# Kernel tuning notes

Hardware: AMD Instinct MI355X
Metric: run time of the kernel (lower is better)

The kernel has to match this reference:

```python
import jax, jax.numpy as jnp
import numpy as np

NUM_FREQ = 10
HIDDEN = 256
ENC_DIM = 2 * 2 * NUM_FREQ  # input_dim * 2 * num_frequencies = 40
OUT_DIM = 3


def setup_inputs() -> dict:
    key = jax.random.key(0)
    ks = jax.random.split(key, 8)
    B, N = 4, 262144
    x = jax.random.uniform(ks[0], (B, N, 2), dtype=jnp.float32)
    # layer 0: enc_dim -> hidden
    W_in = jax.random.normal(ks[1], (ENC_DIM, HIDDEN), dtype=jnp.float32) * (1.0 / np.sqrt(ENC_DIM))
    b_in = jnp.zeros((HIDDEN,), dtype=jnp.float32)
    # layers 1..6: hidden -> hidden (6 of them)
    W_hid = jax.random.normal(ks[2], (6, HIDDEN, HIDDEN), dtype=jnp.float32) * (1.0 / np.sqrt(HIDDEN))
    b_hid = jnp.zeros((6, HIDDEN), dtype=jnp.float32)
    # layer 7: hidden -> out
    W_out = jax.random.normal(ks[3], (HIDDEN, OUT_DIM), dtype=jnp.float32) * (1.0 / np.sqrt(HIDDEN))
    b_out = jnp.zeros((OUT_DIM,), dtype=jnp.float32)
    return {"x": x, "W_in": W_in, "b_in": b_in, "W_hid": W_hid,
            "b_hid": b_hid, "W_out": W_out, "b_out": b_out}


def _pos_encode(x):
    # x: (B, N, 2) -> (B, N, 40). Matches torch: cat([sin, cos], -1) over freq axis then flatten.
    freq = 2.0 ** jnp.arange(NUM_FREQ, dtype=jnp.float32)  # (10,)
    xe = x[..., :, None] * freq  # (B, N, 2, 10)
    enc = jnp.concatenate([jnp.sin(xe), jnp.cos(xe)], axis=-1)  # (B, N, 2, 20)
    return enc.reshape(x.shape[0], x.shape[1], -1)  # (B, N, 40)


def reference(x, W_in, b_in, W_hid, b_hid, W_out, b_out):
    h = _pos_encode(x)
    h = jax.nn.relu(h @ W_in + b_in)
    for i in range(W_hid.shape[0]):  # 6 hidden layers, fixed small loop
        h = jax.nn.relu(h @ W_hid[i] + b_hid[i])
    out = jnp.tanh(h @ W_out + b_out) / 100.0
    return out
```

## Files before the change

kernel.cpp:

```cpp
#include <hip/hip_runtime.h>
#include <stdint.h>

#define THREADS 256
#define BR      128

#define NG_STRIDE 204800
#define WS_WOUT   819200
#define WS_TOTAL  (WS_WOUT + 16384)


typedef short bf16x8 __attribute__((ext_vector_type(8)));
typedef short bf16x4 __attribute__((ext_vector_type(4)));
typedef float f32x16 __attribute__((ext_vector_type(16)));
typedef float f32x4v __attribute__((ext_vector_type(4)));

__device__ __forceinline__ unsigned short f2bf(float f) {
    union { float f; unsigned int u; } v; v.f = f;
    unsigned int u = v.u;
    u += 0x7fffu + ((u >> 16) & 1u);
    return (unsigned short)(u >> 16);
}
__device__ __forceinline__ unsigned int cvt_pk_bf16(float lo, float hi) {
    unsigned int d;
    asm("v_cvt_pk_bf16_f32 %0, %1, %2" : "=v"(d) : "v"(lo), "v"(hi));
    return d;
}
__device__ __forceinline__ bf16x8 ld_act2(const unsigned char* lo,
                                          const unsigned char* hi) {
    bf16x4 a = *(const bf16x4*)lo;
    bf16x4 b = *(const bf16x4*)hi;
    return __builtin_shufflevector(a, b, 0, 1, 2, 3, 4, 5, 6, 7);
}

__global__ void prep_kernel(const float* __restrict__ W_in,
                            const float* __restrict__ W_hid,
                            const float* __restrict__ W_out,
                            unsigned char* __restrict__ ws) {
    int id = blockIdx.x * 256 + threadIdx.x;
    if (id < 16384) {
        int n = id & 255, k = id >> 8;
        int ng = n >> 6, ft = (n >> 5) & 1, ln = n & 31;
        int kk = k >> 4, hi = (k >> 3) & 1, e = k & 7;
        float v = (k < 40) ? W_in[k * 256 + n] : 0.f;
        *(unsigned short*)(ws + ng * NG_STRIDE + (kk * 2 + ft) * 1024
                           + (hi * 32 + ln) * 16 + e * 2) = f2bf(v);
    } else if (id < 16384 + 393216) {
        int e2 = id - 16384;
        int l = e2 >> 16, r = e2 & 65535;
        int k = r >> 8, n = r & 255;
        int c = k >> 6, kk = (k >> 4) & 3, hi = (k >> 3) & 1, e = k & 7;
        int ng = n >> 6, ft = (n >> 5) & 1, ln = n & 31;
        float v = W_hid[l * 65536 + k * 256 + n];
        *(unsigned short*)(ws + ng * NG_STRIDE + 8192 + l * 32768
                           + ((c * 4 + kk) * 2 + ft) * 1024
                           + (hi * 32 + ln) * 16 + e * 2) = f2bf(v);
    } else if (id < 16384 + 393216 + 8192) {
        int e3 = id - 16384 - 393216;
        int n = e3 >> 8, k = e3 & 255;
        int kk = k >> 4, hi = (k >> 3) & 1, e = k & 7;
        float v = (n < 3) ? W_out[k * 3 + n] : 0.f;
        *(unsigned short*)(ws + WS_WOUT + kk * 1024
                           + (hi * 32 + n) * 16 + e * 2) = f2bf(v);
    }
}

__device__ __forceinline__ void bias_init(const float* __restrict__ bp,
                                          f32x16 (&acc)[2][4], int nblk, int hi) {
    #pragma unroll
    for (int tn = 0; tn < 2; ++tn) {
        #pragma unroll
        for (int g4 = 0; g4 < 4; ++g4) {
            f32x4v bv = *(const f32x4v*)(bp + nblk + tn * 32 + g4 * 8 + hi * 4);
            #pragma unroll
            for (int tr = 0; tr < 4; ++tr) {
                #pragma unroll
                for (int j = 0; j < 4; ++j)
                    acc[tn][tr][g4 * 4 + j] = bv[j];
            }
        }
    }
}

__device__ __forceinline__ void epilogue_frag(f32x16 (&acc)[2][4],
                                              unsigned char* actL,
                                              int vW, int wv) {
    #pragma unroll
    for (int tr = 0; tr < 4; ++tr) {
        #pragma unroll
        for (int tn = 0; tn < 2; ++tn) {
            #pragma unroll
            for (int g4 = 0; g4 < 4; ++g4) {
                float v0 = fmaxf(acc[tn][tr][g4 * 4 + 0], 0.f);
                float v1 = fmaxf(acc[tn][tr][g4 * 4 + 1], 0.f);
                float v2 = fmaxf(acc[tn][tr][g4 * 4 + 2], 0.f);
                float v3 = fmaxf(acc[tn][tr][g4 * 4 + 3], 0.f);
                const int ks  = wv * 4 + tn * 2 + (g4 >> 1);
                const int off = (ks * 4 + tr) * 1024 + ((g4 & 1) << 9);
                uint2 u; u.x = cvt_pk_bf16(v0, v1); u.y = cvt_pk_bf16(v2, v3);
                *(uint2*)&actL[vW + off] = u;
            }
        }
    }
}

__global__ __launch_bounds__(THREADS, 2)
void nerf_main(const float* __restrict__ x,
               const float* __restrict__ b_in,
               const float* __restrict__ b_hid,
               const float* __restrict__ b_out,
               const unsigned char* __restrict__ ws,
               float* __restrict__ out, int nrows) {
    __shared__ __align__(16) unsigned char actL[65536];

    const int tid  = threadIdx.x;
    const int lane = tid & 63;
    const int wv   = tid >> 6;
    const int l31  = lane & 31;
    const int hi   = lane >> 5;
    const int hi16 = hi << 4;
    const int rswz  = (l31 & 15) << 3;
    const int rswz2 = rswz ^ 8;
    const int nblk = wv * 64;
    const int gr0  = blockIdx.x * BR;

    const int vB = lane * 16;
    const int vW = l31 * 16 + hi * 8;

    #pragma unroll
    for (int pass = 0; pass < 2; ++pass) {
        const int rr = (tid >> 2) + pass * 64;
        const int part = tid & 3;
        const int co = part >> 1, hf = part & 1;
        const int grow = gr0 + rr;
        float xv = (grow < nrows) ? x[(size_t)grow * 2 + co] : 0.f;
        const int rowo = rr * 512;
        const int rsw = (rr & 15) << 3;
        const int kb = co * 20 + hf * 10;
        float vv[10];
        #pragma unroll
        for (int f = 0; f < 10; ++f) {
            float ang = xv * (float)(1 << f);
            vv[f] = hf ? __cosf(ang) : __sinf(ang);
        }
        #pragma unroll
        for (int p = 0; p < 5; ++p) {
            unsigned int u = cvt_pk_bf16(vv[2 * p], vv[2 * p + 1]);
            int byte = (kb + 2 * p) * 2;
            *(unsigned int*)&actL[rowo + (byte ^ rsw)] = u;
        }
        int z = 80 + part * 12;
        *(unsigned int*)&actL[rowo + ((z    ) ^ rsw)] = 0u;
        *(unsigned int*)&actL[rowo + ((z + 4) ^ rsw)] = 0u;
        *(unsigned int*)&actL[rowo + ((z + 8) ^ rsw)] = 0u;
    }
    __syncthreads();

    f32x16 acc[2][4];
    const unsigned char* wstream = ws + wv * NG_STRIDE + lane * 16;

    {
        bias_init(b_in, acc, nblk, hi);
        int olo[4], ohi[4];
        #pragma unroll
        for (int kk = 0; kk < 4; ++kk) {
            const int bo = kk * 32 + hi16;
            olo[kk] = l31 * 512 + (bo ^ rswz);
            ohi[kk] = l31 * 512 + (bo ^ rswz2);
        }
        __builtin_amdgcn_s_setprio(1);
        #pragma unroll
        for (int kk = 0; kk < 4; ++kk) {
            const unsigned char* fp = wstream + kk * 2048;
            bf16x8 a0 = *(const bf16x8*)(fp);
            bf16x8 a1 = *(const bf16x8*)(fp + 1024);
            #pragma unroll
            for (int tr = 0; tr < 4; ++tr) {
                bf16x8 b = ld_act2(&actL[olo[kk] + tr * 16384],
                                   &actL[ohi[kk] + tr * 16384]);
                acc[0][tr] = __builtin_amdgcn_mfma_f32_32x32x16_bf16(a0, b, acc[0][tr], 0, 0, 0);
                acc[1][tr] = __builtin_amdgcn_mfma_f32_32x32x16_bf16(a1, b, acc[1][tr], 0, 0, 0);
            }
        }
        __builtin_amdgcn_s_setprio(0);
        __syncthreads();
        epilogue_frag(acc, actL, vW, wv);
        __syncthreads();
        wstream += 8192;
    }

    #pragma unroll 1
    for (int l = 0; l < 6; ++l) {
        bias_init(b_hid + l * 256, acc, nblk, hi);
        __builtin_amdgcn_s_setprio(1);
        #pragma unroll
        for (int c = 0; c < 4; ++c) {
            #pragma unroll
            for (int kk = 0; kk < 4; ++kk) {
                const unsigned char* fp = wstream + (c * 4 + kk) * 2048;
                bf16x8 a0 = *(const bf16x8*)(fp);
                bf16x8 a1 = *(const bf16x8*)(fp + 1024);
                const int fo = (c * 4 + kk) * 4096;
                #pragma unroll
                for (int tr = 0; tr < 4; ++tr) {
                    bf16x8 b = *(const bf16x8*)&actL[vB + fo + tr * 1024];
                    acc[0][tr] = __builtin_amdgcn_mfma_f32_32x32x16_bf16(a0, b, acc[0][tr], 0, 0, 0);
                    acc[1][tr] = __builtin_amdgcn_mfma_f32_32x32x16_bf16(a1, b, acc[1][tr], 0, 0, 0);
                }
            }
        }
        __builtin_amdgcn_s_setprio(0);
        __syncthreads();
        epilogue_frag(acc, actL, vW, wv);
        __syncthreads();
        wstream += 32768;
    }

    {
        f32x16 c0, c1;
        #pragma unroll
        for (int j = 0; j < 16; ++j) { c0[j] = 0.f; c1[j] = 0.f; }
        const unsigned char* wo = ws + WS_WOUT + lane * 16;
        #pragma unroll
        for (int kk = 0; kk < 16; ++kk) {
            bf16x8 a = *(const bf16x8*)(wo + kk * 1024);
            bf16x8 b = *(const bf16x8*)&actL[vB + (kk * 4 + wv) * 1024];
            if (kk & 1) c1 = __builtin_amdgcn_mfma_f32_32x32x16_bf16(a, b, c1, 0, 0, 0);
            else        c0 = __builtin_amdgcn_mfma_f32_32x32x16_bf16(a, b, c0, 0, 0, 0);
        }
        if (hi == 0) {
            const int row = gr0 + wv * 32 + l31;
            if (row < nrows) {
                float* op = out + (size_t)row * 3;
                #pragma unroll
                for (int j = 0; j < 3; ++j)
                    op[j] = tanhf(c0[j] + c1[j] + b_out[j]) * 0.01f;
            }
        }
    }
}

extern "C" void kernel_launch(void* const* d_in, const int* in_sizes, int n_in,
                              void* d_out, int out_size, void* d_ws, size_t ws_size,
                              hipStream_t stream) {
    (void)n_in; (void)out_size;
    const float* x     = (const float*)d_in[0];
    const float* W_in  = (const float*)d_in[1];
    const float* b_in  = (const float*)d_in[2];
    const float* W_hid = (const float*)d_in[3];
    const float* b_hid = (const float*)d_in[4];
    const float* W_out = (const float*)d_in[5];
    const float* b_out = (const float*)d_in[6];
    unsigned char* ws  = (unsigned char*)d_ws;
    float* out = (float*)d_out;

    if (ws_size < (size_t)WS_TOTAL) return;

    const int nrows = in_sizes[0] / 2;
    const int grid  = (nrows + BR - 1) / BR;

    prep_kernel<<<1632, 256, 0, stream>>>(W_in, W_hid, W_out, ws);
    nerf_main<<<grid, THREADS, 0, stream>>>(x, b_in, b_hid, b_out, ws, out, nrows);
}
```

Measured before the change: 716.7 us.

## Use 512-thread blocks of 64 rows with ping-pong activation buffers

Blocks shrink from 128 rows to 64 and grow from 256 to 512 threads. Eight waves split into 4 column groups times 2 row groups, each wave accumulating a single 32-row tile instead of four. Activations alternate between two LDS halves across layers, which removes the barrier before each epilogue. This lowers register pressure (launch bounds 4) for higher occupancy, but each weight fragment fetched from global memory now feeds fewer MFMAs, so per-row weight traffic roughly doubles.

```diff
diff --git a/kernel.cpp b/kernel.cpp
--- a/kernel.cpp
+++ b/kernel.cpp
@@ -1,8 +1,8 @@
 #include <hip/hip_runtime.h>
 #include <stdint.h>
 
-#define THREADS 256
-#define BR      128
+#define THREADS 512
+#define BR      64
 
 #define NG_STRIDE 204800
 #define WS_WOUT   819200
@@ -65,45 +65,65 @@
 }
 
 __device__ __forceinline__ void bias_init(const float* __restrict__ bp,
-                                          f32x16 (&acc)[2][4], int nblk, int hi) {
+                                          f32x16 (&acc)[2], int nblk, int hi) {
     #pragma unroll
     for (int tn = 0; tn < 2; ++tn) {
         #pragma unroll
         for (int g4 = 0; g4 < 4; ++g4) {
             f32x4v bv = *(const f32x4v*)(bp + nblk + tn * 32 + g4 * 8 + hi * 4);
             #pragma unroll
-            for (int tr = 0; tr < 4; ++tr) {
-                #pragma unroll
-                for (int j = 0; j < 4; ++j)
-                    acc[tn][tr][g4 * 4 + j] = bv[j];
-            }
-        }
-    }
-}
-
-__device__ __forceinline__ void epilogue_frag(f32x16 (&acc)[2][4],
+            for (int j = 0; j < 4; ++j)
+                acc[tn][g4 * 4 + j] = bv[j];
+        }
+    }
+}
+
+template <int WBO>
+__device__ __forceinline__ void epilogue_frag(f32x16 (&acc)[2],
                                               unsigned char* actL,
-                                              int vW, int wv) {
+                                              int vW, int ng) {
     #pragma unroll
-    for (int tr = 0; tr < 4; ++tr) {
-        #pragma unroll
-        for (int tn = 0; tn < 2; ++tn) {
-            #pragma unroll
-            for (int g4 = 0; g4 < 4; ++g4) {
-                float v0 = fmaxf(acc[tn][tr][g4 * 4 + 0], 0.f);
-                float v1 = fmaxf(acc[tn][tr][g4 * 4 + 1], 0.f);
-                float v2 = fmaxf(acc[tn][tr][g4 * 4 + 2], 0.f);
-                float v3 = fmaxf(acc[tn][tr][g4 * 4 + 3], 0.f);
-                const int ks  = wv * 4 + tn * 2 + (g4 >> 1);
-                const int off = (ks * 4 + tr) * 1024 + ((g4 & 1) << 9);
-                uint2 u; u.x = cvt_pk_bf16(v0, v1); u.y = cvt_pk_bf16(v2, v3);
-                *(uint2*)&actL[vW + off] = u;
-            }
-        }
-    }
-}
-
-__global__ __launch_bounds__(THREADS, 2)
+    for (int tn = 0; tn < 2; ++tn) {
+        #pragma unroll
+        for (int g4 = 0; g4 < 4; ++g4) {
+            float v0 = fmaxf(acc[tn][g4 * 4 + 0], 0.f);
+            float v1 = fmaxf(acc[tn][g4 * 4 + 1], 0.f);
+            float v2 = fmaxf(acc[tn][g4 * 4 + 2], 0.f);
+            float v3 = fmaxf(acc[tn][g4 * 4 + 3], 0.f);
+            const int ks  = ng * 4 + tn * 2 + (g4 >> 1);
+            const int off = WBO + ks * 2048 + ((g4 & 1) << 9);
+            uint2 u; u.x = cvt_pk_bf16(v0, v1); u.y = cvt_pk_bf16(v2, v3);
+            *(uint2*)&actL[vW + off] = u;
+        }
+    }
+}
+
+template <int RBO, int WBO>
+__device__ __forceinline__ void hidden_layer(const unsigned char* __restrict__ wl,
+                                             const float* __restrict__ bp,
+                                             unsigned char* actL, f32x16 (&acc)[2],
+                                             int vB, int vW, int ng,
+                                             int nblk, int hi) {
+    bias_init(bp, acc, nblk, hi);
+    __builtin_amdgcn_s_setprio(1);
+    #pragma unroll
+    for (int c = 0; c < 4; ++c) {
+        #pragma unroll
+        for (int kk = 0; kk < 4; ++kk) {
+            const unsigned char* fp = wl + (c * 4 + kk) * 2048;
+            bf16x8 a0 = *(const bf16x8*)(fp);
+            bf16x8 a1 = *(const bf16x8*)(fp + 1024);
+            bf16x8 b  = *(const bf16x8*)&actL[vB + RBO + (c * 4 + kk) * 2048];
+            acc[0] = __builtin_amdgcn_mfma_f32_32x32x16_bf16(a0, b, acc[0], 0, 0, 0);
+            acc[1] = __builtin_amdgcn_mfma_f32_32x32x16_bf16(a1, b, acc[1], 0, 0, 0);
+        }
+    }
+    __builtin_amdgcn_s_setprio(0);
+    epilogue_frag<WBO>(acc, actL, vW, ng);
+    __syncthreads();
+}
+
+__global__ __launch_bounds__(THREADS, 4)
 void nerf_main(const float* __restrict__ x,
                const float* __restrict__ b_in,
                const float* __restrict__ b_hid,
@@ -115,20 +135,21 @@
     const int tid  = threadIdx.x;
     const int lane = tid & 63;
     const int wv   = tid >> 6;
+    const int ng   = wv & 3;
+    const int rg   = wv >> 2;
     const int l31  = lane & 31;
     const int hi   = lane >> 5;
     const int hi16 = hi << 4;
     const int rswz  = (l31 & 15) << 3;
     const int rswz2 = rswz ^ 8;
-    const int nblk = wv * 64;
+    const int nblk = ng * 64;
     const int gr0  = blockIdx.x * BR;
 
-    const int vB = lane * 16;
-    const int vW = l31 * 16 + hi * 8;
-
-    #pragma unroll
-    for (int pass = 0; pass < 2; ++pass) {
-        const int rr = (tid >> 2) + pass * 64;
+    const int vB = lane * 16 + rg * 1024;
+    const int vW = l31 * 16 + hi * 8 + rg * 1024;
+
+    if (tid < 256) {
+        const int rr = tid >> 2;
         const int part = tid & 3;
         const int co = part >> 1, hf = part & 1;
         const int grow = gr0 + rr;
@@ -155,67 +176,41 @@
     }
     __syncthreads();
 
-    f32x16 acc[2][4];
-    const unsigned char* wstream = ws + wv * NG_STRIDE + lane * 16;
+    f32x16 acc[2];
+    const unsigned char* wstream = ws + ng * NG_STRIDE + lane * 16;
 
     {
         bias_init(b_in, acc, nblk, hi);
-        int olo[4], ohi[4];
-        #pragma unroll
-        for (int kk = 0; kk < 4; ++kk) {
-            const int bo = kk * 32 + hi16;
-            olo[kk] = l31 * 512 + (bo ^ rswz);
-            ohi[kk] = l31 * 512 + (bo ^ rswz2);
-        }
         __builtin_amdgcn_s_setprio(1);
         #pragma unroll
         for (int kk = 0; kk < 4; ++kk) {
             const unsigned char* fp = wstream + kk * 2048;
             bf16x8 a0 = *(const bf16x8*)(fp);
             bf16x8 a1 = *(const bf16x8*)(fp + 1024);
-            #pragma unroll
-            for (int tr = 0; tr < 4; ++tr) {
-                bf16x8 b = ld_act2(&actL[olo[kk] + tr * 16384],
-                                   &actL[ohi[kk] + tr * 16384]);
-                acc[0][tr] = __builtin_amdgcn_mfma_f32_32x32x16_bf16(a0, b, acc[0][tr], 0, 0, 0);
-                acc[1][tr] = __builtin_amdgcn_mfma_f32_32x32x16_bf16(a1, b, acc[1][tr], 0, 0, 0);
-            }
+            const int bo = kk * 32 + hi16;
+            const int ro = rg * 16384 + l31 * 512;
+            bf16x8 b = ld_act2(&actL[ro + (bo ^ rswz)],
+                               &actL[ro + (bo ^ rswz2)]);
+            acc[0] = __builtin_amdgcn_mfma_f32_32x32x16_bf16(a0, b, acc[0], 0, 0, 0);
+            acc[1] = __builtin_amdgcn_mfma_f32_32x32x16_bf16(a1, b, acc[1], 0, 0, 0);
         }
         __builtin_amdgcn_s_setprio(0);
-        __syncthreads();
-        epilogue_frag(acc, actL, vW, wv);
+        epilogue_frag<32768>(acc, actL, vW, ng);
         __syncthreads();
         wstream += 8192;
     }
 
     #pragma unroll 1
-    for (int l = 0; l < 6; ++l) {
-        bias_init(b_hid + l * 256, acc, nblk, hi);
-        __builtin_amdgcn_s_setprio(1);
-        #pragma unroll
-        for (int c = 0; c < 4; ++c) {
-            #pragma unroll
-            for (int kk = 0; kk < 4; ++kk) {
-                const unsigned char* fp = wstream + (c * 4 + kk) * 2048;
-                bf16x8 a0 = *(const bf16x8*)(fp);
-                bf16x8 a1 = *(const bf16x8*)(fp + 1024);
-                const int fo = (c * 4 + kk) * 4096;
-                #pragma unroll
-                for (int tr = 0; tr < 4; ++tr) {
-                    bf16x8 b = *(const bf16x8*)&actL[vB + fo + tr * 1024];
-                    acc[0][tr] = __builtin_amdgcn_mfma_f32_32x32x16_bf16(a0, b, acc[0][tr], 0, 0, 0);
-                    acc[1][tr] = __builtin_amdgcn_mfma_f32_32x32x16_bf16(a1, b, acc[1][tr], 0, 0, 0);
-                }
-            }
-        }
-        __builtin_amdgcn_s_setprio(0);
-        __syncthreads();
-        epilogue_frag(acc, actL, vW, wv);
-        __syncthreads();
+    for (int p = 0; p < 3; ++p) {
+        hidden_layer<32768, 0>(wstream, b_hid + (2 * p) * 256,
+                               actL, acc, vB, vW, ng, nblk, hi);
         wstream += 32768;
-    }
-
-    {
+        hidden_layer<0, 32768>(wstream, b_hid + (2 * p + 1) * 256,
+                               actL, acc, vB, vW, ng, nblk, hi);
+        wstream += 32768;
+    }
+
+    if (wv < 2) {
         f32x16 c0, c1;
         #pragma unroll
         for (int j = 0; j < 16; ++j) { c0[j] = 0.f; c1[j] = 0.f; }
@@ -223,7 +218,7 @@
         #pragma unroll
         for (int kk = 0; kk < 16; ++kk) {
             bf16x8 a = *(const bf16x8*)(wo + kk * 1024);
-            bf16x8 b = *(const bf16x8*)&actL[vB + (kk * 4 + wv) * 1024];
+            bf16x8 b = *(const bf16x8*)&actL[32768 + lane * 16 + (kk * 2 + wv) * 1024];
             if (kk & 1) c1 = __builtin_amdgcn_mfma_f32_32x32x16_bf16(a, b, c1, 0, 0, 0);
             else        c0 = __builtin_amdgcn_mfma_f32_32x32x16_bf16(a, b, c0, 0, 0, 0);
         }
```

New measurement: 1.082 ms. 50.9% more time.

## Halve row tile to 64 and raise occupancy to three blocks per CU

Applied to the files above, without the earlier changes.

Cuts the rows per block from 128 to 64. This halves the accumulator registers and the LDS activation buffer (to 32 KB), so the launch bound can rise to three blocks per CU. The activation layout strides and the output-layer wave assignment are changed to match. __syncthreads is swapped for an explicit lgkmcnt wait plus s_barrier. The trade-off is that each weight fragment loaded from global/L2 now feeds half as many MFMAs, which doubles weight traffic per row.

```diff
diff --git a/kernel.cpp b/kernel.cpp
--- a/kernel.cpp
+++ b/kernel.cpp
@@ -2,7 +2,7 @@
 #include <stdint.h>
 
 #define THREADS 256
-#define BR      128
+#define BR      64
 
 #define NG_STRIDE 204800
 #define WS_WOUT   819200
@@ -30,6 +30,10 @@
     bf16x4 a = *(const bf16x4*)lo;
     bf16x4 b = *(const bf16x4*)hi;
     return __builtin_shufflevector(a, b, 0, 1, 2, 3, 4, 5, 6, 7);
+}
+__device__ __forceinline__ void lds_barrier() {
+    asm volatile("s_waitcnt lgkmcnt(0)" ::: "memory");
+    __builtin_amdgcn_s_barrier();
 }
 
 __global__ void prep_kernel(const float* __restrict__ W_in,
@@ -65,14 +69,14 @@
 }
 
 __device__ __forceinline__ void bias_init(const float* __restrict__ bp,
-                                          f32x16 (&acc)[2][4], int nblk, int hi) {
+                                          f32x16 (&acc)[2][2], int nblk, int hi) {
     #pragma unroll
     for (int tn = 0; tn < 2; ++tn) {
         #pragma unroll
         for (int g4 = 0; g4 < 4; ++g4) {
             f32x4v bv = *(const f32x4v*)(bp + nblk + tn * 32 + g4 * 8 + hi * 4);
             #pragma unroll
-            for (int tr = 0; tr < 4; ++tr) {
+            for (int tr = 0; tr < 2; ++tr) {
                 #pragma unroll
                 for (int j = 0; j < 4; ++j)
                     acc[tn][tr][g4 * 4 + j] = bv[j];
@@ -81,11 +85,11 @@
     }
 }
 
-__device__ __forceinline__ void epilogue_frag(f32x16 (&acc)[2][4],
+__device__ __forceinline__ void epilogue_frag(f32x16 (&acc)[2][2],
                                               unsigned char* actL,
                                               int vW, int wv) {
     #pragma unroll
-    for (int tr = 0; tr < 4; ++tr) {
+    for (int tr = 0; tr < 2; ++tr) {
         #pragma unroll
         for (int tn = 0; tn < 2; ++tn) {
             #pragma unroll
@@ -95,7 +99,7 @@
                 float v2 = fmaxf(acc[tn][tr][g4 * 4 + 2], 0.f);
                 float v3 = fmaxf(acc[tn][tr][g4 * 4 + 3], 0.f);
                 const int ks  = wv * 4 + tn * 2 + (g4 >> 1);
-                const int off = (ks * 4 + tr) * 1024 + ((g4 & 1) << 9);
+                const int off = (ks * 2 + tr) * 1024 + ((g4 & 1) << 9);
                 uint2 u; u.x = cvt_pk_bf16(v0, v1); u.y = cvt_pk_bf16(v2, v3);
                 *(uint2*)&actL[vW + off] = u;
             }
@@ -103,14 +107,40 @@
     }
 }
 
-__global__ __launch_bounds__(THREADS, 2)
+__device__ __forceinline__ void hidden_layer(const unsigned char* __restrict__ wl,
+                                             const float* __restrict__ bp,
+                                             unsigned char* actL, f32x16 (&acc)[2][2],
+                                             int vB, int vW, int wv,
+                                             int nblk, int hi) {
+    bias_init(bp, acc, nblk, hi);
+    __builtin_amdgcn_s_setprio(1);
+    #pragma unroll
+    for (int s = 0; s < 16; ++s) {
+        const unsigned char* fp = wl + s * 2048;
+        bf16x8 a0 = *(const bf16x8*)(fp);
+        bf16x8 a1 = *(const bf16x8*)(fp + 1024);
+        const int fo = s * 2048;
+        #pragma unroll
+        for (int tr = 0; tr < 2; ++tr) {
+            bf16x8 b = *(const bf16x8*)&actL[vB + fo + tr * 1024];
+            acc[0][tr] = __builtin_amdgcn_mfma_f32_32x32x16_bf16(a0, b, acc[0][tr], 0, 0, 0);
+            acc[1][tr] = __builtin_amdgcn_mfma_f32_32x32x16_bf16(a1, b, acc[1][tr], 0, 0, 0);
+        }
+    }
+    __builtin_amdgcn_s_setprio(0);
+    lds_barrier();
+    epilogue_frag(acc, actL, vW, wv);
+    lds_barrier();
+}
+
+__global__ __launch_bounds__(THREADS, 3)
 void nerf_main(const float* __restrict__ x,
                const float* __restrict__ b_in,
                const float* __restrict__ b_hid,
                const float* __restrict__ b_out,
                const unsigned char* __restrict__ ws,
                float* __restrict__ out, int nrows) {
-    __shared__ __align__(16) unsigned char actL[65536];
+    __shared__ __align__(16) unsigned char actL[32768];
 
     const int tid  = threadIdx.x;
     const int lane = tid & 63;
@@ -126,9 +156,8 @@
     const int vB = lane * 16;
     const int vW = l31 * 16 + hi * 8;
 
-    #pragma unroll
-    for (int pass = 0; pass < 2; ++pass) {
-        const int rr = (tid >> 2) + pass * 64;
+    {
+        const int rr = tid >> 2;
         const int part = tid & 3;
         const int co = part >> 1, hf = part & 1;
         const int grow = gr0 + rr;
@@ -155,7 +184,7 @@
     }
     __syncthreads();
 
-    f32x16 acc[2][4];
+    f32x16 acc[2][2];
     const unsigned char* wstream = ws + wv * NG_STRIDE + lane * 16;
 
     {
@@ -174,7 +203,7 @@
             bf16x8 a0 = *(const bf16x8*)(fp);
             bf16x8 a1 = *(const bf16x8*)(fp + 1024);
             #pragma unroll
-            for (int tr = 0; tr < 4; ++tr) {
+            for (int tr = 0; tr < 2; ++tr) {
                 bf16x8 b = ld_act2(&actL[olo[kk] + tr * 16384],
                                    &actL[ohi[kk] + tr * 16384]);
                 acc[0][tr] = __builtin_amdgcn_mfma_f32_32x32x16_bf16(a0, b, acc[0][tr], 0, 0, 0);
@@ -182,40 +211,20 @@
             }
         }
         __builtin_amdgcn_s_setprio(0);
-        __syncthreads();
+        lds_barrier();
         epilogue_frag(acc, actL, vW, wv);
-        __syncthreads();
+        lds_barrier();
         wstream += 8192;
     }
 
     #pragma unroll 1
     for (int l = 0; l < 6; ++l) {
-        bias_init(b_hid + l * 256, acc, nblk, hi);
-        __builtin_amdgcn_s_setprio(1);
-        #pragma unroll
-        for (int c = 0; c < 4; ++c) {
-            #pragma unroll
-            for (int kk = 0; kk < 4; ++kk) {
-                const unsigned char* fp = wstream + (c * 4 + kk) * 2048;
-                bf16x8 a0 = *(const bf16x8*)(fp);
-                bf16x8 a1 = *(const bf16x8*)(fp + 1024);
-                const int fo = (c * 4 + kk) * 4096;
-                #pragma unroll
-                for (int tr = 0; tr < 4; ++tr) {
-                    bf16x8 b = *(const bf16x8*)&actL[vB + fo + tr * 1024];
-                    acc[0][tr] = __builtin_amdgcn_mfma_f32_32x32x16_bf16(a0, b, acc[0][tr], 0, 0, 0);
-                    acc[1][tr] = __builtin_amdgcn_mfma_f32_32x32x16_bf16(a1, b, acc[1][tr], 0, 0, 0);
-                }
-            }
-        }
-        __builtin_amdgcn_s_setprio(0);
-        __syncthreads();
-        epilogue_frag(acc, actL, vW, wv);
-        __syncthreads();
+        hidden_layer(wstream, b_hid + l * 256,
+                     actL, acc, vB, vW, wv, nblk, hi);
         wstream += 32768;
     }
 
-    {
+    if (wv < 2) {
         f32x16 c0, c1;
         #pragma unroll
         for (int j = 0; j < 16; ++j) { c0[j] = 0.f; c1[j] = 0.f; }
@@ -223,7 +232,7 @@
         #pragma unroll
         for (int kk = 0; kk < 16; ++kk) {
             bf16x8 a = *(const bf16x8*)(wo + kk * 1024);
-            bf16x8 b = *(const bf16x8*)&actL[vB + (kk * 4 + wv) * 1024];
+            bf16x8 b = *(const bf16x8*)&actL[vB + (kk * 2 + wv) * 1024];
             if (kk & 1) c1 = __builtin_amdgcn_mfma_f32_32x32x16_bf16(a, b, c1, 0, 0, 0);
             else        c0 = __builtin_amdgcn_mfma_f32_32x32x16_bf16(a, b, c0, 0, 0, 0);
         }
```

New measurement: 805.4 us (median of 3 runs). 12.4% more time.
